# Performance work log

Hardware: AMD Instinct MI355X
Metric: run time of the kernel (lower is better)

Reference implementation:

```python
import jax, jax.numpy as jnp
import numpy as np
from functools import partial

TAU = 2.0       # membrane time constant
V_TH = 1.0      # firing threshold
SLOPE = 10.0    # surrogate sigmoid slope (matches rate_encode's 10*)
T = 10          # time_window
H = 12          # num_heads


def lif_step(v, I):
    """One LIF update: leaky integrate, surrogate spike, multiplicative reset."""
    v = v + (I - v) / TAU
    spk = jax.nn.sigmoid(SLOPE * (v - V_TH))
    v = v * (1.0 - spk)
    return spk, v


def setup_inputs() -> dict:
    key = jax.random.key(0)
    ks = jax.random.split(key, 5)
    B, S, E = 8, 1024, 768
    scale = 1.0 / np.sqrt(E)
    x = jax.random.uniform(ks[0], (B, S, E), dtype=jnp.float32)
    Wq = jax.random.normal(ks[1], (E, E), dtype=jnp.float32) * scale
    Wk = jax.random.normal(ks[2], (E, E), dtype=jnp.float32) * scale
    Wv = jax.random.normal(ks[3], (E, E), dtype=jnp.float32) * scale
    Wo = jax.random.normal(ks[4], (E, E), dtype=jnp.float32) * scale
    zb = jnp.zeros((E,), dtype=jnp.float32)
    return {"x": x, "Wq": Wq, "bq": zb, "Wk": Wk, "bk": zb,
            "Wv": Wv, "bv": zb, "Wo": Wo, "bo": zb}


def reference(x, Wq, bq, Wk, bk, Wv, bv, Wo, bo):
    B, S, E = x.shape
    D = E // H
    # rate encoding probability (x assumed in [0,1] range, clipped)
    p = jnp.clip(x, 0.0, 1.0)  # [B,S,E]

    def step(carry, t):
        vq, vk, vv, Qa, Ka, Va = carry
        inp = jax.nn.sigmoid(SLOPE * (p * T - t))  # [B,S,E] spikes at step t
        qs, vq = lif_step(vq, inp @ Wq.T + bq)
        ks, vk = lif_step(vk, inp @ Wk.T + bk)
        vs, vv = lif_step(vv, inp @ Wv.T + bv)
        return (vq, vk, vv, Qa + qs, Ka + ks, Va + vs), None

    z = jnp.zeros((B, S, E), dtype=x.dtype)
    t_idx = jnp.arange(T, dtype=x.dtype)
    (vq, vk, vv, Q, K, V), _ = jax.lax.scan(step, (z, z, z, z, z, z), t_idx)

    # split heads: [B,S,E] -> [B,H,S,D]
    Qh = Q.reshape(B, S, H, D)
    Kh = K.reshape(B, S, H, D)
    Vh = V.reshape(B, S, H, D)
    scores = jnp.einsum('bqhd,bkhd->bhqk', Qh, Kh) / np.sqrt(D)
    attn = jax.nn.softmax(scores, axis=-1)
    out_h = jnp.einsum('bhqk,bkhd->bqhd', attn, Vh)  # [B,S,H,D]
    out = out_h.reshape(B, S, E)
    # output LIF projection with fresh (zero) state
    out_spk, _ = lif_step(jnp.zeros_like(out), out @ Wo.T + bo)
    return out_spk
```

## Files before the change

### kernel.cpp

```cpp
#include <hip/hip_runtime.h>
#include <math.h>

constexpr int B_ = 8, S_ = 1024, E_ = 768, H_ = 12, D_ = 64, T_ = 10;
constexpr int N_ = B_ * S_;
constexpr int NE_ = N_ * E_;
constexpr int WE_ = E_ * E_;

typedef __attribute__((ext_vector_type(8))) short bf16x8;
typedef __attribute__((ext_vector_type(4))) float f32x4;

#define MFMA16(a,b,c) __builtin_amdgcn_mfma_f32_16x16x32_bf16(a,b,c,0,0,0)

__device__ __forceinline__ float sigm(float z){ return 1.f/(1.f+__expf(-z)); }
__device__ __forceinline__ unsigned short f2bf(float f){
    unsigned int u = __float_as_uint(f);
    u += 0x7FFFu + ((u>>16)&1u);
    return (unsigned short)(u>>16);
}
__device__ __forceinline__ float bf2f(unsigned short h){
    return __uint_as_float(((unsigned int)h)<<16);
}
__device__ __forceinline__ void gl16(const void* g, void* l){
    __builtin_amdgcn_global_load_lds((const __attribute__((address_space(1))) unsigned int*)g,
                                     (__attribute__((address_space(3))) unsigned int*)l, 16, 0, 0);
}

__global__ __launch_bounds__(256) void encode_k(const float* __restrict__ x,
                                                unsigned short* __restrict__ enc){
    const int i = blockIdx.x*256 + threadIdx.x;
    const float4 a = ((const float4*)x)[2*i];
    const float4 b = ((const float4*)x)[2*i+1];
    float p[8] = {a.x,a.y,a.z,a.w,b.x,b.y,b.z,b.w};
#pragma unroll
    for (int e=0;e<8;++e) p[e] = 100.f*fminf(fmaxf(p[e],0.f),1.f);
#pragma unroll
    for (int t=0;t<T_;++t){
        unsigned int w[4];
#pragma unroll
        for (int e=0;e<4;++e){
            unsigned short u0 = f2bf(sigm(p[2*e]   - 10.f*(float)t));
            unsigned short u1 = f2bf(sigm(p[2*e+1] - 10.f*(float)t));
            w[e] = (unsigned int)u0 | ((unsigned int)u1<<16);
        }
        ((uint4*)(enc + (long)t*NE_))[i] = make_uint4(w[0],w[1],w[2],w[3]);
    }
}

__global__ __launch_bounds__(256) void wsplit_k(const float* __restrict__ Wq, const float* __restrict__ Wk,
        const float* __restrict__ Wv, const float* __restrict__ Wo,
        unsigned short* __restrict__ whi, unsigned short* __restrict__ wlo){
    int gi = blockIdx.x*256 + threadIdx.x;
    int z = gi / (WE_/8);
    int r = gi % (WE_/8);
    const float* W = z==0?Wq : z==1?Wk : z==2?Wv : Wo;
    const float4 a = ((const float4*)W)[2*r];
    const float4 b = ((const float4*)W)[2*r+1];
    float f[8]={a.x,a.y,a.z,a.w,b.x,b.y,b.z,b.w};
    unsigned int h[4], l[4];
#pragma unroll
    for (int e=0;e<4;++e){
        unsigned short h0=f2bf(f[2*e]),   l0=f2bf(f[2*e]  -bf2f(h0));
        unsigned short h1=f2bf(f[2*e+1]), l1=f2bf(f[2*e+1]-bf2f(h1));
        h[e] = (unsigned)h0 | ((unsigned)h1<<16);
        l[e] = (unsigned)l0 | ((unsigned)l1<<16);
    }
    ((uint4*)(whi + (long)z*WE_))[r] = make_uint4(h[0],h[1],h[2],h[3]);
    ((uint4*)(wlo + (long)z*WE_))[r] = make_uint4(l[0],l[1],l[2],l[3]);
}

__global__ __launch_bounds__(256,3) void qkv_k(const unsigned short* __restrict__ enc,
        const unsigned short* __restrict__ whi,
        const float* __restrict__ bq, const float* __restrict__ bk, const float* __restrict__ bv,
        float* __restrict__ Qf, float* __restrict__ Kf, float* __restrict__ Vf){
    const int bid = blockIdx.x;
    const int xcd = bid & 7;
    const int lb  = bid >> 3;
    const int rt  = xcd*8 + lb/36;
    const int cz  = lb % 36;
    const int z   = cz / 12;
    const int ct  = cz % 12;
    const unsigned short* Wh = whi + (long)z*WE_;
    const float* bias = z==0?bq : z==1?bk : bv;
    float* Out = z==0?Qf : z==1?Kf : Vf;
    const int row0 = rt*128, col0 = ct*64;

    __shared__ unsigned short Ab[2][128*64];
    __shared__ unsigned short Bh[2][64*64];

    const int tid = threadIdx.x, lane = tid&63, wid = tid>>6;
    const int l15 = lane&15, l4 = lane>>4, l7 = lane&7;
    const int wr = wid>>1, wc = wid&1;

    int aSrc[4], bSrc[2];
#pragma unroll
    for (int s=0;s<4;++s){
        int idx = (wid + s*4)*64 + lane;
        int row = idx>>3, ch = idx&7;
        aSrc[s] = (row0+row)*E_ + ((ch ^ (row&7))<<3);
    }
#pragma unroll
    for (int s=0;s<2;++s){
        int idx = (wid + s*4)*64 + lane;
        int row = idx>>3, ch = idx&7;
        bSrc[s] = (col0+row)*E_ + ((ch ^ (row&7))<<3);
    }

    const int aBase = (wr*64 + l15)*128;
    const int bBase = (wc*32 + l15)*128;
    const int sw[2] = { ((l4^l7)<<4), ((((4+l4))^l7)<<4) };

    f32x4 acc[4][2];
    float vm[4][2][4] = {};
    float qa[4][2][4] = {};
    float bn[2];
#pragma unroll
    for (int n=0;n<2;++n) bn[n] = bias[col0 + wc*32 + n*16 + l15];
    asm volatile("" :: "v"(bn[0]), "v"(bn[1]));

    const f32x4 zero4 = {0.f,0.f,0.f,0.f};

#define STAGE(tt, kk2, slot)                                               \
    do {                                                                   \
        const unsigned short* eb_ = enc + (long)(tt)*NE_ + (kk2)*64;       \
        _Pragma("unroll")                                                  \
        for (int s_=0;s_<4;++s_)                                           \
            gl16(eb_ + aSrc[s_], &Ab[slot][(wid+s_*4)*512]);               \
        _Pragma("unroll")                                                  \
        for (int s_=0;s_<2;++s_)                                           \
            gl16(Wh + bSrc[s_] + (kk2)*64, &Bh[slot][(wid+s_*4)*512]);     \
    } while(0)

    STAGE(0, 0, 0);

    for (int t=0;t<T_;++t){
#pragma unroll
        for (int m=0;m<4;++m)
#pragma unroll
            for (int n=0;n<2;++n) acc[m][n] = zero4;
#pragma unroll
        for (int kt=0;kt<12;++kt){
            const int slotC = kt&1;
            const int slotS = slotC^1;
            if (kt < 11){
                STAGE(t, kt+1, slotS);
                asm volatile("s_waitcnt vmcnt(6)" ::: "memory");
            } else if (t < 9){
                STAGE(t+1, 0, slotS);
                asm volatile("s_waitcnt vmcnt(6)" ::: "memory");
            } else {
                asm volatile("s_waitcnt vmcnt(0)" ::: "memory");
            }
            __builtin_amdgcn_s_barrier();
            __builtin_amdgcn_s_setprio(1);
#pragma unroll
            for (int kk=0;kk<2;++kk){
                bf16x8 af[4], fbh[2];
#pragma unroll
                for (int m=0;m<4;++m)
                    af[m] = *(const bf16x8*)((const char*)&Ab[slotC][0] + aBase + m*2048 + sw[kk]);
#pragma unroll
                for (int n=0;n<2;++n)
                    fbh[n] = *(const bf16x8*)((const char*)&Bh[slotC][0] + bBase + n*2048 + sw[kk]);
#pragma unroll
                for (int m=0;m<4;++m)
#pragma unroll
                    for (int n=0;n<2;++n)
                        acc[m][n] = MFMA16(af[m], fbh[n], acc[m][n]);
            }
            __builtin_amdgcn_s_setprio(0);
            __builtin_amdgcn_s_barrier();
        }
#pragma unroll
        for (int m=0;m<4;++m)
#pragma unroll
            for (int n=0;n<2;++n)
#pragma unroll
                for (int j=0;j<4;++j){
                    float I = acc[m][n][j] + bn[n];
                    float v = (vm[m][n][j] + I)*0.5f;
                    float s = sigm(10.f*v - 10.f);
                    vm[m][n][j] = v*(1.f - s);
                    qa[m][n][j] += s;
                }
    }
#undef STAGE
#pragma unroll
    for (int m=0;m<4;++m)
#pragma unroll
        for (int n=0;n<2;++n)
#pragma unroll
            for (int j=0;j<4;++j){
                int row = row0 + wr*64 + m*16 + l4*4 + j;
                int col = col0 + wc*32 + n*16 + l15;
                Out[(long)row*E_ + col] = qa[m][n][j];
            }
}

__global__ __launch_bounds__(256,2) void attn_k2(const float* __restrict__ Qf, const float* __restrict__ Kf,
        const float* __restrict__ Vf, unsigned short* __restrict__ atth, unsigned short* __restrict__ attl){
    const int bid = blockIdx.x;
    const int xcd = bid & 7;
    const int vb  = bid >> 3;
    const int q0  = (vb & 15) * 64;
    const int bhg = xcd*12 + (vb >> 4);
    const int h   = bhg % 12;
    const int b   = bhg / 12;
    const long base = ((long)b*S_)*E_ + h*64;

    __shared__ char smem[65536];
    unsigned short* Qh = (unsigned short*)(smem);
    unsigned short* Ql = (unsigned short*)(smem + 8192);
    unsigned short* Kh = (unsigned short*)(smem + 16384);
    unsigned short* Kl = (unsigned short*)(smem + 24576);
    unsigned short* Vh = (unsigned short*)(smem + 32768);
    unsigned short* Vl = (unsigned short*)(smem + 40960);
    unsigned short* Ph = (unsigned short*)(smem + 49152);
    unsigned short* Pl = (unsigned short*)(smem + 57344);
    float* OT = (float*)(smem + 16384);

    const int tid = threadIdx.x, lane = tid&63, wid = tid>>6;
    const int l15 = lane&15, l4 = lane>>4, l7 = lane&7;
    const int qrow = wid*16 + l15;

    {
        int q = tid>>2, c0 = (tid&3)*2;
        const float* src = Qf + base + (long)(q0+q)*E_ + (tid&3)*16;
        float4 f0=((const float4*)src)[0], f1=((const float4*)src)[1];
        float4 f2=((const float4*)src)[2], f3=((const float4*)src)[3];
        float f[16]={f0.x,f0.y,f0.z,f0.w,f1.x,f1.y,f1.z,f1.w,f2.x,f2.y,f2.z,f2.w,f3.x,f3.y,f3.z,f3.w};
        bf16x8 vh[2], vl[2];
#pragma unroll
        for (int g=0;g<2;++g)
#pragma unroll
            for (int e=0;e<8;++e){
                unsigned short hh = f2bf(f[g*8+e]);
                vh[g][e] = (short)hh;
                vl[g][e] = (short)f2bf(f[g*8+e]-bf2f(hh));
            }
        int by0 = q*128 + (((c0  ) ^ (q&7))<<4);
        int by1 = q*128 + (((c0+1) ^ (q&7))<<4);
        *(bf16x8*)((char*)Qh + by0) = vh[0];
        *(bf16x8*)((char*)Qh + by1) = vh[1];
        *(bf16x8*)((char*)Ql + by0) = vl[0];
        *(bf16x8*)((char*)Ql + by1) = vl[1];
    }
    __syncthreads();
    bf16x8 qfh[2], qfl[2];
#pragma unroll
    for (int kk=0;kk<2;++kk){
        int off = qrow*128 + ((((kk<<2)+l4) ^ l7)<<4);
        qfh[kk] = *(const bf16x8*)((const char*)Qh + off);
        qfl[kk] = *(const bf16x8*)((const char*)Ql + off);
    }

    float mrun = -1e30f, lrun = 0.f;
    f32x4 ot[4];
    const f32x4 zero4 = {0.f,0.f,0.f,0.f};
#pragma unroll
    for (int m=0;m<4;++m) ot[m] = zero4;

    for (int kt=0;kt<16;++kt){
        const int k0 = kt*64;
        __syncthreads();
        {
            int key = tid>>2, c0 = (tid&3)*2;
            const float* src = Kf + base + (long)(k0+key)*E_ + (tid&3)*16;
            float4 f0=((const float4*)src)[0], f1=((const float4*)src)[1];
            float4 f2=((const float4*)src)[2], f3=((const float4*)src)[3];
            float f[16]={f0.x,f0.y,f0.z,f0.w,f1.x,f1.y,f1.z,f1.w,f2.x,f2.y,f2.z,f2.w,f3.x,f3.y,f3.z,f3.w};
            bf16x8 vh[2], vl[2];
#pragma unroll
            for (int g=0;g<2;++g)
#pragma unroll
                for (int e=0;e<8;++e){
                    unsigned short hh = f2bf(f[g*8+e]);
                    vh[g][e] = (short)hh;
                    vl[g][e] = (short)f2bf(f[g*8+e]-bf2f(hh));
                }
            int by0 = key*128 + (((c0  ) ^ (key&7))<<4);
            int by1 = key*128 + (((c0+1) ^ (key&7))<<4);
            *(bf16x8*)((char*)Kh + by0) = vh[0];
            *(bf16x8*)((char*)Kh + by1) = vh[1];
            *(bf16x8*)((char*)Kl + by0) = vl[0];
            *(bf16x8*)((char*)Kl + by1) = vl[1];
        }
#pragma unroll
        for (int rr=0;rr<2;++rr){
            int dq = (tid>>5) + rr*8;
            int kp = tid&31;
            const float* s0 = Vf + base + (long)(k0 + 2*kp)*E_ + dq*4;
            float4 va = *(const float4*)s0;
            float4 vb = *(const float4*)(s0 + E_);
            float fa[4]={va.x,va.y,va.z,va.w}, fb[4]={vb.x,vb.y,vb.z,vb.w};
#pragma unroll
            for (int dd=0;dd<4;++dd){
                int d = dq*4+dd;
                unsigned short ha=f2bf(fa[dd]), hb=f2bf(fb[dd]);
                unsigned short la=f2bf(fa[dd]-bf2f(ha)), lb=f2bf(fb[dd]-bf2f(hb));
                int byte = d*128 + ((kp<<2) ^ ((d&7)<<4));
                *(unsigned int*)((char*)Vh + byte) = (unsigned)ha | ((unsigned)hb<<16);
                *(unsigned int*)((char*)Vl + byte) = (unsigned)la | ((unsigned)lb<<16);
            }
        }
        __syncthreads();
        f32x4 st[4];
#pragma unroll
        for (int m=0;m<4;++m) st[m] = zero4;
#pragma unroll
        for (int kk=0;kk<2;++kk){
            int swo = ((((kk<<2)+l4) ^ l7)<<4);
            bf16x8 kh[4], kl2[4];
#pragma unroll
            for (int m=0;m<4;++m){
                int off = (m*16+l15)*128 + swo;
                kh[m]  = *(const bf16x8*)((const char*)Kh + off);
                kl2[m] = *(const bf16x8*)((const char*)Kl + off);
            }
#pragma unroll
            for (int m=0;m<4;++m){
                st[m] = MFMA16(kh[m],  qfh[kk], st[m]);
                st[m] = MFMA16(kh[m],  qfl[kk], st[m]);
                st[m] = MFMA16(kl2[m], qfh[kk], st[m]);
            }
        }
        float pmax = -1e30f;
#pragma unroll
        for (int m=0;m<4;++m)
#pragma unroll
            for (int j=0;j<4;++j){ st[m][j] *= 0.125f; pmax = fmaxf(pmax, st[m][j]); }
        pmax = fmaxf(pmax, __shfl_xor(pmax,16));
        pmax = fmaxf(pmax, __shfl_xor(pmax,32));
        float mnew = fmaxf(mrun, pmax);
        float alpha = __expf(mrun - mnew);
        float p[16]; float psum = 0.f;
#pragma unroll
        for (int m=0;m<4;++m)
#pragma unroll
            for (int j=0;j<4;++j){ float e = __expf(st[m][j]-mnew); p[m*4+j]=e; psum+=e; }
        psum += __shfl_xor(psum,16);
        psum += __shfl_xor(psum,32);
        lrun = lrun*alpha + psum;
        mrun = mnew;
#pragma unroll
        for (int m=0;m<4;++m)
#pragma unroll
            for (int j=0;j<4;++j) ot[m][j] *= alpha;
#pragma unroll
        for (int m=0;m<4;++m)
#pragma unroll
            for (int jp=0;jp<2;++jp){
                float fx = p[m*4+jp*2], fy = p[m*4+jp*2+1];
                unsigned short hx=f2bf(fx), hy=f2bf(fy);
                unsigned short lx=f2bf(fx-bf2f(hx)), ly=f2bf(fy-bf2f(hy));
                int key = m*16 + l4*4 + jp*2;
                int byte = qrow*128 + ((key<<1) ^ (l7<<4));
                *(unsigned int*)((char*)Ph + byte) = (unsigned)hx | ((unsigned)hy<<16);
                *(unsigned int*)((char*)Pl + byte) = (unsigned)lx | ((unsigned)ly<<16);
            }
#pragma unroll
        for (int kk=0;kk<2;++kk){
            int swo = ((((kk<<2)+l4) ^ l7)<<4);
            bf16x8 pfh = *(const bf16x8*)((const char*)Ph + qrow*128 + swo);
            bf16x8 pfl = *(const bf16x8*)((const char*)Pl + qrow*128 + swo);
#pragma unroll
            for (int m=0;m<4;++m){
                int off = (m*16+l15)*128 + swo;
                bf16x8 vvh = *(const bf16x8*)((const char*)Vh + off);
                bf16x8 vvl = *(const bf16x8*)((const char*)Vl + off);
                ot[m] = MFMA16(vvh, pfh, ot[m]);
                ot[m] = MFMA16(vvh, pfl, ot[m]);
                ot[m] = MFMA16(vvl, pfh, ot[m]);
            }
        }
    }
    __syncthreads();
    float inv = 1.f/lrun;
#pragma unroll
    for (int m=0;m<4;++m)
#pragma unroll
        for (int j=0;j<4;++j){
            int d = m*16 + l4*4 + j;
            OT[qrow*68 + d] = ot[m][j]*inv;
        }
    __syncthreads();
    {
        int q = tid>>2, d0 = (tid&3)*16;
        const float* rp = OT + q*68 + d0;
        float4 f0=((const float4*)rp)[0], f1=((const float4*)rp)[1];
        float4 f2=((const float4*)rp)[2], f3=((const float4*)rp)[3];
        float f[16]={f0.x,f0.y,f0.z,f0.w,f1.x,f1.y,f1.z,f1.w,f2.x,f2.y,f2.z,f2.w,f3.x,f3.y,f3.z,f3.w};
        bf16x8 vh[2], vl[2];
#pragma unroll
        for (int g=0;g<2;++g)
#pragma unroll
            for (int e=0;e<8;++e){
                unsigned short hh = f2bf(f[g*8+e]);
                vh[g][e] = (short)hh;
                vl[g][e] = (short)f2bf(f[g*8+e]-bf2f(hh));
            }
        long o = base + (long)(q0+q)*E_ + d0;
        *(bf16x8*)(atth + o)     = vh[0];
        *(bf16x8*)(atth + o + 8) = vh[1];
        *(bf16x8*)(attl + o)     = vl[0];
        *(bf16x8*)(attl + o + 8) = vl[1];
    }
}

__global__ __launch_bounds__(256,2) void out_k(const unsigned short* __restrict__ Ah_g,
        const unsigned short* __restrict__ Al_g,
        const unsigned short* __restrict__ Wh, const unsigned short* __restrict__ Wl,
        const float* __restrict__ bias, float* __restrict__ out){
    const int row0 = blockIdx.x*128, col0 = blockIdx.y*64;
    __shared__ unsigned short Ah[128*64], Al[128*64];
    __shared__ unsigned short Bh2[64*64], Bl2[64*64];

    const int tid = threadIdx.x, lane = tid&63, wid = tid>>6;
    const int l15 = lane&15, l4 = lane>>4, l7 = lane&7;
    const int wr = wid>>1, wc = wid&1;

    int aSrc[4], bSrc[2];
#pragma unroll
    for (int s=0;s<4;++s){
        int idx = (wid + s*4)*64 + lane;
        int row = idx>>3, ch = idx&7;
        aSrc[s] = (row0+row)*E_ + ((ch ^ (row&7))<<3);
    }
#pragma unroll
    for (int s=0;s<2;++s){
        int idx = (wid + s*4)*64 + lane;
        int row = idx>>3, ch = idx&7;
        bSrc[s] = (col0+row)*E_ + ((ch ^ (row&7))<<3);
    }
    const int aBase = (wr*64 + l15)*128;
    const int bBase = (wc*32 + l15)*128;
    const int sw[2] = { ((l4^l7)<<4), ((((4+l4))^l7)<<4) };

    f32x4 acc[4][2];
    const f32x4 zero4 = {0.f,0.f,0.f,0.f};
#pragma unroll
    for (int m=0;m<4;++m)
#pragma unroll
        for (int n=0;n<2;++n) acc[m][n] = zero4;

    for (int kt=0;kt<12;++kt){
        const int k0 = kt*64;
        __syncthreads();
#pragma unroll
        for (int s=0;s<4;++s){
            gl16(Ah_g + aSrc[s] + k0, &Ah[(wid+s*4)*512]);
            gl16(Al_g + aSrc[s] + k0, &Al[(wid+s*4)*512]);
        }
#pragma unroll
        for (int s=0;s<2;++s){
            gl16(Wh + bSrc[s] + k0, &Bh2[(wid+s*4)*512]);
            gl16(Wl + bSrc[s] + k0, &Bl2[(wid+s*4)*512]);
        }
        __syncthreads();
#pragma unroll
        for (int kk=0;kk<2;++kk){
            bf16x8 ah[4], al[4], fbh[2], fbl[2];
#pragma unroll
            for (int m=0;m<4;++m){
                ah[m] = *(const bf16x8*)((const char*)Ah + aBase + m*2048 + sw[kk]);
                al[m] = *(const bf16x8*)((const char*)Al + aBase + m*2048 + sw[kk]);
            }
#pragma unroll
            for (int n=0;n<2;++n){
                fbh[n] = *(const bf16x8*)((const char*)Bh2 + bBase + n*2048 + sw[kk]);
                fbl[n] = *(const bf16x8*)((const char*)Bl2 + bBase + n*2048 + sw[kk]);
            }
#pragma unroll
            for (int m=0;m<4;++m)
#pragma unroll
                for (int n=0;n<2;++n){
                    acc[m][n] = MFMA16(ah[m], fbh[n], acc[m][n]);
                    acc[m][n] = MFMA16(ah[m], fbl[n], acc[m][n]);
                    acc[m][n] = MFMA16(al[m], fbh[n], acc[m][n]);
                }
        }
    }
#pragma unroll
    for (int m=0;m<4;++m)
#pragma unroll
        for (int n=0;n<2;++n){
            float bn = bias[col0 + wc*32 + n*16 + l15];
#pragma unroll
            for (int j=0;j<4;++j){
                int row = row0 + wr*64 + m*16 + l4*4 + j;
                int col = col0 + wc*32 + n*16 + l15;
                float I = acc[m][n][j] + bn;
                out[(long)row*E_ + col] = sigm(5.f*I - 10.f);
            }
        }
}

extern "C" void kernel_launch(void* const* d_in, const int* in_sizes, int n_in,
                              void* d_out, int out_size, void* d_ws, size_t ws_size,
                              hipStream_t stream){
    const float* x  = (const float*)d_in[0];
    const float* Wq = (const float*)d_in[1];
    const float* bq = (const float*)d_in[2];
    const float* Wk = (const float*)d_in[3];
    const float* bk = (const float*)d_in[4];
    const float* Wv = (const float*)d_in[5];
    const float* bv = (const float*)d_in[6];
    const float* Wo = (const float*)d_in[7];
    const float* bo = (const float*)d_in[8];
    float* out = (float*)d_out;

    char* ws = (char*)d_ws;
    unsigned short* enc  = (unsigned short*)ws;
    unsigned short* atth = (unsigned short*)ws;
    unsigned short* attl = (unsigned short*)(ws + (long)NE_*2);
    unsigned short* whi  = (unsigned short*)(ws + 125829120L);
    unsigned short* wlo  = whi + 4L*WE_;
    float* Qf = (float*)(ws + 135266304L);
    float* Kf = Qf + NE_;
    float* Vf = Kf + NE_;

    wsplit_k<<<dim3(4*(WE_/8)/256), 256, 0, stream>>>(Wq,Wk,Wv,Wo,whi,wlo);
    encode_k<<<dim3(NE_/8/256), 256, 0, stream>>>(x,enc);
    qkv_k<<<dim3(2304), 256, 0, stream>>>(enc,whi,bq,bk,bv,Qf,Kf,Vf);
    attn_k2<<<dim3(1536), 256, 0, stream>>>(Qf,Kf,Vf,atth,attl);
    out_k<<<dim3(64,12), 256, 0, stream>>>(atth,attl,whi+3L*WE_,wlo+3L*WE_,bo,out);
}
```

Measured before the change: 726.6 us.

## Widen QKV tile to 128x128 and remap block-to-XCD swizzle

```diff
diff --git a/kernel.cpp b/kernel.cpp
--- a/kernel.cpp
+++ b/kernel.cpp
@@ -68,54 +68,49 @@
     ((uint4*)(wlo + (long)z*WE_))[r] = make_uint4(l[0],l[1],l[2],l[3]);
 }
 
-__global__ __launch_bounds__(256,3) void qkv_k(const unsigned short* __restrict__ enc,
+__global__ __launch_bounds__(256,2) void qkv_k(const unsigned short* __restrict__ enc,
         const unsigned short* __restrict__ whi,
         const float* __restrict__ bq, const float* __restrict__ bk, const float* __restrict__ bv,
         float* __restrict__ Qf, float* __restrict__ Kf, float* __restrict__ Vf){
     const int bid = blockIdx.x;
-    const int xcd = bid & 7;
-    const int lb  = bid >> 3;
-    const int rt  = xcd*8 + lb/36;
-    const int cz  = lb % 36;
-    const int z   = cz / 12;
-    const int ct  = cz % 12;
+    const int xcd = (bid>>3)&7;
+    const int u   = ((bid>>6)<<3) | (bid&7);
+    const int rt  = xcd*8 + u/18;
+    const int cz  = u%18;
+    const int z   = cz/6;
+    const int ct  = cz%6;
     const unsigned short* Wh = whi + (long)z*WE_;
     const float* bias = z==0?bq : z==1?bk : bv;
     float* Out = z==0?Qf : z==1?Kf : Vf;
-    const int row0 = rt*128, col0 = ct*64;
+    const int row0 = rt*128, col0 = ct*128;
 
     __shared__ unsigned short Ab[2][128*64];
-    __shared__ unsigned short Bh[2][64*64];
+    __shared__ unsigned short Bb[2][128*64];
 
     const int tid = threadIdx.x, lane = tid&63, wid = tid>>6;
     const int l15 = lane&15, l4 = lane>>4, l7 = lane&7;
     const int wr = wid>>1, wc = wid&1;
 
-    int aSrc[4], bSrc[2];
+    int aSrc[4], bSrc[4];
 #pragma unroll
     for (int s=0;s<4;++s){
         int idx = (wid + s*4)*64 + lane;
         int row = idx>>3, ch = idx&7;
         aSrc[s] = (row0+row)*E_ + ((ch ^ (row&7))<<3);
-    }
-#pragma unroll
-    for (int s=0;s<2;++s){
-        int idx = (wid + s*4)*64 + lane;
-        int row = idx>>3, ch = idx&7;
         bSrc[s] = (col0+row)*E_ + ((ch ^ (row&7))<<3);
     }
 
     const int aBase = (wr*64 + l15)*128;
-    const int bBase = (wc*32 + l15)*128;
+    const int bBase = (wc*64 + l15)*128;
     const int sw[2] = { ((l4^l7)<<4), ((((4+l4))^l7)<<4) };
 
-    f32x4 acc[4][2];
-    float vm[4][2][4] = {};
-    float qa[4][2][4] = {};
-    float bn[2];
-#pragma unroll
-    for (int n=0;n<2;++n) bn[n] = bias[col0 + wc*32 + n*16 + l15];
-    asm volatile("" :: "v"(bn[0]), "v"(bn[1]));
+    f32x4 acc[4][4];
+    float vm[4][4][4] = {};
+    float qa[4][4][4] = {};
+    float bn[4];
+#pragma unroll
+    for (int n=0;n<4;++n) bn[n] = bias[col0 + wc*64 + n*16 + l15];
+    asm volatile("" :: "v"(bn[0]), "v"(bn[1]), "v"(bn[2]), "v"(bn[3]));
 
     const f32x4 zero4 = {0.f,0.f,0.f,0.f};
 
@@ -123,11 +118,10 @@
     do {                                                                   \
         const unsigned short* eb_ = enc + (long)(tt)*NE_ + (kk2)*64;       \
         _Pragma("unroll")                                                  \
-        for (int s_=0;s_<4;++s_)                                           \
+        for (int s_=0;s_<4;++s_){                                          \
             gl16(eb_ + aSrc[s_], &Ab[slot][(wid+s_*4)*512]);               \
-        _Pragma("unroll")                                                  \
-        for (int s_=0;s_<2;++s_)                                           \
-            gl16(Wh + bSrc[s_] + (kk2)*64, &Bh[slot][(wid+s_*4)*512]);     \
+            gl16(Wh + bSrc[s_] + (kk2)*64, &Bb[slot][(wid+s_*4)*512]);     \
+        }                                                                  \
     } while(0)
 
     STAGE(0, 0, 0);
@@ -136,17 +130,17 @@
 #pragma unroll
         for (int m=0;m<4;++m)
 #pragma unroll
-            for (int n=0;n<2;++n) acc[m][n] = zero4;
+            for (int n=0;n<4;++n) acc[m][n] = zero4;
 #pragma unroll
         for (int kt=0;kt<12;++kt){
             const int slotC = kt&1;
             const int slotS = slotC^1;
             if (kt < 11){
                 STAGE(t, kt+1, slotS);
-                asm volatile("s_waitcnt vmcnt(6)" ::: "memory");
+                asm volatile("s_waitcnt vmcnt(8)" ::: "memory");
             } else if (t < 9){
                 STAGE(t+1, 0, slotS);
-                asm volatile("s_waitcnt vmcnt(6)" ::: "memory");
+                asm volatile("s_waitcnt vmcnt(8)" ::: "memory");
             } else {
                 asm volatile("s_waitcnt vmcnt(0)" ::: "memory");
             }
@@ -154,18 +148,18 @@
             __builtin_amdgcn_s_setprio(1);
 #pragma unroll
             for (int kk=0;kk<2;++kk){
-                bf16x8 af[4], fbh[2];
+                bf16x8 af[4], fb[4];
 #pragma unroll
                 for (int m=0;m<4;++m)
                     af[m] = *(const bf16x8*)((const char*)&Ab[slotC][0] + aBase + m*2048 + sw[kk]);
 #pragma unroll
-                for (int n=0;n<2;++n)
-                    fbh[n] = *(const bf16x8*)((const char*)&Bh[slotC][0] + bBase + n*2048 + sw[kk]);
+                for (int n=0;n<4;++n)
+                    fb[n] = *(const bf16x8*)((const char*)&Bb[slotC][0] + bBase + n*2048 + sw[kk]);
 #pragma unroll
                 for (int m=0;m<4;++m)
 #pragma unroll
-                    for (int n=0;n<2;++n)
-                        acc[m][n] = MFMA16(af[m], fbh[n], acc[m][n]);
+                    for (int n=0;n<4;++n)
+                        acc[m][n] = MFMA16(af[m], fb[n], acc[m][n]);
             }
             __builtin_amdgcn_s_setprio(0);
             __builtin_amdgcn_s_barrier();
@@ -173,7 +167,7 @@
 #pragma unroll
         for (int m=0;m<4;++m)
 #pragma unroll
-            for (int n=0;n<2;++n)
+            for (int n=0;n<4;++n)
 #pragma unroll
                 for (int j=0;j<4;++j){
                     float I = acc[m][n][j] + bn[n];
@@ -187,11 +181,11 @@
 #pragma unroll
     for (int m=0;m<4;++m)
 #pragma unroll
-        for (int n=0;n<2;++n)
+        for (int n=0;n<4;++n)
 #pragma unroll
             for (int j=0;j<4;++j){
                 int row = row0 + wr*64 + m*16 + l4*4 + j;
-                int col = col0 + wc*32 + n*16 + l15;
+                int col = col0 + wc*64 + n*16 + l15;
                 Out[(long)row*E_ + col] = qa[m][n][j];
             }
 }
@@ -199,10 +193,10 @@
 __global__ __launch_bounds__(256,2) void attn_k2(const float* __restrict__ Qf, const float* __restrict__ Kf,
         const float* __restrict__ Vf, unsigned short* __restrict__ atth, unsigned short* __restrict__ attl){
     const int bid = blockIdx.x;
-    const int xcd = bid & 7;
-    const int vb  = bid >> 3;
-    const int q0  = (vb & 15) * 64;
-    const int bhg = xcd*12 + (vb >> 4);
+    const int xcd = (bid>>3)&7;
+    const int u   = ((bid>>6)<<3) | (bid&7);
+    const int q0  = (u & 15) * 64;
+    const int bhg = xcd*12 + (u >> 4);
     const int h   = bhg % 12;
     const int b   = bhg / 12;
     const long base = ((long)b*S_)*E_ + h*64;
@@ -520,7 +514,7 @@
 
     wsplit_k<<<dim3(4*(WE_/8)/256), 256, 0, stream>>>(Wq,Wk,Wv,Wo,whi,wlo);
     encode_k<<<dim3(NE_/8/256), 256, 0, stream>>>(x,enc);
-    qkv_k<<<dim3(2304), 256, 0, stream>>>(enc,whi,bq,bk,bv,Qf,Kf,Vf);
+    qkv_k<<<dim3(1152), 256, 0, stream>>>(enc,whi,bq,bk,bv,Qf,Kf,Vf);
     attn_k2<<<dim3(1536), 256, 0, stream>>>(Qf,Kf,Vf,atth,attl);
     out_k<<<dim3(64,12), 256, 0, stream>>>(atth,attl,whi+3L*WE_,wlo+3L*WE_,bo,out);
 }
```

Result: slower. 1.034 ms (+42.3%).
